# Kernel tuning notes

Hardware: AMD Instinct MI355X
Metric: run time of the kernel (lower is better)

The kernel has to match this reference:

```python
import jax, jax.numpy as jnp
import numpy as np

DIM = 64
NUM_HEAD = 4
C_IN = 2 * DIM                      # dim * proj_ratio
N_PER_HEAD = C_IN // NUM_HEAD       # 32
M_TRI = N_PER_HEAD * (N_PER_HEAD + 1) // 2   # 528
C_POOL = NUM_HEAD * M_TRI           # 2112 == dim*(dim+2)/2
EPS = 1e-5


def setup_inputs() -> dict:
    key = jax.random.key(0)
    ks = jax.random.split(key, 8)
    B, H, W = 4, 128, 128
    x = jax.random.normal(ks[0], (B, C_IN, H, W), dtype=jnp.float32)
    norm1_w = 1.0 + 0.1 * jax.random.normal(ks[1], (C_IN,), dtype=jnp.float32)
    norm1_b = 0.1 * jax.random.normal(ks[2], (C_IN,), dtype=jnp.float32)
    dr_w = 0.02 * jax.random.normal(ks[3], (DIM, C_POOL), dtype=jnp.float32)
    dr_b = 0.02 * jax.random.normal(ks[4], (DIM,), dtype=jnp.float32)
    norm2_w = 1.0 + 0.1 * jax.random.normal(ks[5], (DIM,), dtype=jnp.float32)
    norm2_b = 0.1 * jax.random.normal(ks[6], (DIM,), dtype=jnp.float32)
    fc1_w = 0.05 * jax.random.normal(ks[7], (DIM, DIM), dtype=jnp.float32)
    fc1_b = jnp.zeros((DIM,), dtype=jnp.float32)
    return {"x": x, "norm1_w": norm1_w, "norm1_b": norm1_b,
            "dr_w": dr_w, "dr_b": dr_b,
            "norm2_w": norm2_w, "norm2_b": norm2_b,
            "fc1_w": fc1_w, "fc1_b": fc1_b}


def _layernorm_nchw(x, g, b):
    # LayerNorm over channel dim of NCHW tensor (torch permutes to NHWC first)
    xt = jnp.transpose(x, (0, 2, 3, 1))
    mu = jnp.mean(xt, axis=-1, keepdims=True)
    var = jnp.mean(jnp.square(xt - mu), axis=-1, keepdims=True)
    y = (xt - mu) / jnp.sqrt(var + EPS) * g + b
    return jnp.transpose(y, (0, 3, 1, 2))


def reference(x, norm1_w, norm1_b, dr_w, dr_b, norm2_w, norm2_b, fc1_w, fc1_b):
    B, C, H, W = x.shape
    L = H * W
    nh, n = NUM_HEAD, N_PER_HEAD

    # --- norm1 ---
    x = _layernorm_nchw(x, norm1_w, norm1_b)

    # --- MHSP ---
    # channel shuffle: group = C // num_head = n, group_C = num_head
    x = x.reshape(B, n, nh, H, W).transpose(0, 2, 1, 3, 4).reshape(B, C, H, W)
    # unfold with kernel=1, stride=1, pad=0 is a pure reshape -> [B, L, C]
    t = x.reshape(B, C, L).transpose(0, 2, 1).reshape(B, L, nh, n)
    # per-position per-head rank-1 outer product: [B, L, nh, n, n]
    outer = jnp.einsum('blhi,blhj->blhij', t, t)
    # sparse_mapping matmul == gather of upper-triangle entries (row-major i<=j)
    iu, ju = np.triu_indices(n)
    pf = outer[..., iu, ju]                      # [B, L, nh, m]
    pf = pf.reshape(B, L, nh * M_TRI).transpose(0, 2, 1).reshape(B, C_POOL, H, W)

    # --- CTM token mixer ---
    C2 = C_POOL
    y = pf.reshape(B, nh, C2 // nh, L)
    yn = y / jnp.linalg.norm(y, axis=2, keepdims=True)
    mid = L // 2
    x0 = yn[..., mid]                            # [B, nh, C2/nh]
    attn = jnp.einsum('bhc,bhcl->bhl', x0, yn)   # [B, nh, L]
    attn = jax.nn.softmax(attn, axis=-1)[:, :, None, :]
    y = (y * attn * float(L)).reshape(B, C2, H, W)

    # --- dimension reduction (1x1 conv) ---
    z = jnp.einsum('bchw,oc->bohw', y, dr_w) + dr_b[None, :, None, None]

    # --- norm2 + LightMlp (1x1 conv + GELU) ---
    z = _layernorm_nchw(z, norm2_w, norm2_b)
    z = jnp.einsum('bchw,oc->bohw', z, fc1_w) + fc1_b[None, :, None, None]
    z = jax.nn.gelu(z, approximate=False)
    return z
```

## Files before the change

### kernel.cpp

```cpp
#include <hip/hip_runtime.h>
#include <hip/hip_bf16.h>
#include <math.h>

#define B_    4
#define CIN   128
#define L_    16384
#define NH    4
#define NN    32
#define MT    528
#define CP    2112
#define DIM_  64
#define LT    64
#define MID   8192
#define EPS_  1e-5f

#define KPH   640
#define KTOT  2560
#define WSWN  (KTOT * DIM_)
#define FSWN  (2 * 4 * 64 * 8)
#define LOGITS_BLOCKS 1024
#define PREP_BLOCKS   656

typedef __attribute__((ext_vector_type(8))) short short8;
typedef __attribute__((ext_vector_type(4))) float float4v;

__device__ inline unsigned short f2bf(float f) {
  unsigned u = __float_as_uint(f);
  unsigned r = (u + 0x7fffu + ((u >> 16) & 1u)) >> 16;
  return (unsigned short)r;
}
__device__ inline float bf2f(unsigned short h) {
  return __uint_as_float(((unsigned)h) << 16);
}

__device__ inline void kb_decode(int id, int& i, int& jb) {
  if (id < 32)      { i = id >> 2;               jb = id & 3; }
  else if (id < 56) { int r = id - 32; int d = r / 3; i = 8 + d;  jb = 1 + (r - 3 * d); }
  else if (id < 72) { int r = id - 56; i = 16 + (r >> 1); jb = 2 + (r & 1); }
  else              { i = 24 + (id - 72);         jb = 3; }
}

__global__ __launch_bounds__(256) void k_pre(const float* __restrict__ dr_w,
                                             const float* __restrict__ fc1_w,
                                             const float* __restrict__ x,
                                             const float* __restrict__ g1,
                                             const float* __restrict__ b1,
                                             unsigned short* __restrict__ wsw,
                                             unsigned short* __restrict__ fsw,
                                             float* __restrict__ ws_a,
                                             float* __restrict__ ws_bsum) {
  if (blockIdx.x >= LOGITS_BLOCKS) {
    int s = (blockIdx.x - LOGITS_BLOCKS) * 256 + threadIdx.x;
    if (s < WSWN) {
      int j    = s & 7;
      int lane = (s >> 3) & 63;
      int ot   = (s >> 9) & 3;
      int ksg  = s >> 11;
      int o  = ot * 16 + (lane & 15);
      int kp = ksg * 32 + (lane >> 4) * 8 + j;
      int h  = kp / KPH;
      int kk = kp - h * KPH;
      int kb = kk >> 3, jo = kk & 7;
      int i, jb; kb_decode(kb, i, jb);
      int jch = jb * 8 + jo;
      float val = 0.f;
      if (jch >= i) {
        int fi = 32 * i - (i * (i - 1)) / 2;
        int m  = h * MT + fi + (jch - i);
        val = dr_w[(size_t)o * CP + m];
      }
      wsw[s] = f2bf(val);
    } else {
      int s2 = s - WSWN;
      int j    = s2 & 7;
      int lane = (s2 >> 3) & 63;
      int ot   = (s2 >> 9) & 3;
      int ks2  = s2 >> 11;
      int o = ot * 16 + (lane & 15);
      int c = ks2 * 32 + (lane >> 4) * 8 + j;
      fsw[s2] = f2bf(fc1_w[o * DIM_ + c]);
    }
    return;
  }
  int blk = blockIdx.x;
  int b = blk >> 8;
  int l0 = (blk & 255) << 6;
  int t = threadIdx.x;
  int l = t & 63, q = t >> 6;
  __shared__ float xs[CIN], smid[CIN];
  __shared__ float part[4][64], part2[4][64], mu_s[64], isd_s[64];
  __shared__ float musd[2];

  if (t < CIN) xs[t] = x[(size_t)b * CIN * L_ + (size_t)t * L_ + MID];

  float tv[32];
  const float* xb = x + (size_t)b * CIN * L_ + l0 + l;
  float s = 0.f, s2 = 0.f;
#pragma unroll
  for (int cc = 0; cc < 32; cc++) {
    float v = xb[(size_t)(cc * 4 + q) * L_];
    tv[cc] = v; s += v; s2 += v * v;
  }
  part[q][l] = s; part2[q][l] = s2;
  __syncthreads();
  if (t == 0) {
    float su = 0.f;
    for (int c = 0; c < CIN; c++) su += xs[c];
    float mu = su / CIN;
    float sv = 0.f;
    for (int c = 0; c < CIN; c++) { float d = xs[c] - mu; sv += d * d; }
    musd[0] = mu; musd[1] = rsqrtf(sv / CIN + EPS_);
  }
  if (t < 64) {
    float su = part[0][t] + part[1][t] + part[2][t] + part[3][t];
    float su2 = part2[0][t] + part2[1][t] + part2[2][t] + part2[3][t];
    float mu = su * (1.f / CIN);
    float var = su2 * (1.f / CIN) - mu * mu;
    mu_s[t] = mu; isd_s[t] = rsqrtf(var + EPS_);
  }
  __syncthreads();
  if (t < CIN) {
    int c = ((t & 31) << 2) + (t >> 5);
    smid[t] = (xs[c] - musd[0]) * musd[1] * g1[c] + b1[c];
  }
  {
    float mu = mu_s[l], isd = isd_s[l];
#pragma unroll
    for (int cc = 0; cc < 32; cc++) {
      int co = cc * 4 + q;
      tv[cc] = (tv[cc] - mu) * isd * g1[co] + b1[co];
    }
  }
  __syncthreads();
  float T2 = 0.f, T4 = 0.f, st = 0.f, sc2 = 0.f, S2 = 0.f, S4 = 0.f;
#pragma unroll
  for (int i = 0; i < 32; i++) {
    float si = smid[q * 32 + i];
    float ti = tv[i];
    float t2 = ti * ti;
    T2 += t2; T4 = fmaf(t2, t2, T4);
    float ci = si * ti;
    st += ci; sc2 = fmaf(ci, ci, sc2);
    float s2i = si * si;
    S2 += s2i; S4 = fmaf(s2i, s2i, S4);
  }
  float num = 0.5f * (st * st + sc2);
  float logit = num * rsqrtf(0.25f * (T2 * T2 + T4) * (S2 * S2 + S4));
  float e = expf(logit - 1.f);
  ws_a[((size_t)b * NH + q) * L_ + l0 + l] = e;
  float ws = e;
#pragma unroll
  for (int mk = 1; mk < 64; mk <<= 1) ws += __shfl_xor(ws, mk, 64);
  if (l == 0) ws_bsum[((size_t)b * NH + q) * 256 + (blk & 255)] = ws;
}

struct __align__(16) SmemM {
  union __align__(16) { unsigned short p2[4 * 5 * 4 * 16 * 8]; float zb[64 * 65]; } u1;
  union __align__(16) { unsigned short ut[64 * 128]; unsigned short zn2[4 * 2 * 4 * 16 * 8]; } u2;
  float part[4][64], part2[4][64], mu_s[64], isd_s[64];
};

__device__ inline int utidx(int l, int c) {
  return l * 128 + ((((c >> 3) ^ (l & 7))) << 3) + (c & 7);
}

__global__ __launch_bounds__(256, 3) void k_main(const float* __restrict__ x,
      const float* __restrict__ g1, const float* __restrict__ b1,
      const float* __restrict__ dr_b,
      const float* __restrict__ g2, const float* __restrict__ b2,
      const float* __restrict__ fc1_b,
      const unsigned short* __restrict__ wsw, const unsigned short* __restrict__ fsw,
      const float* __restrict__ ws_a, const float* __restrict__ ws_bsum,
      float* __restrict__ out) {
  __shared__ SmemM sm;
  int blk = blockIdx.x;
  int b = blk >> 8;
  int l0 = (blk & 255) << 6;
  int t = threadIdx.x;
  int l = t & 63, q = t >> 6;

  float asum;
  {
    const float* bs = ws_bsum + ((size_t)b * NH + q) * 256;
    float a0 = bs[l] + bs[l + 64] + bs[l + 128] + bs[l + 192];
#pragma unroll
    for (int mk = 1; mk < 64; mk <<= 1) a0 += __shfl_xor(a0, mk, 64);
    asum = a0;
  }
  float e = ws_a[((size_t)b * NH + q) * L_ + l0 + l];
  float sa = sqrtf(e * ((float)L_ / asum));

  const float* xb = x + (size_t)b * CIN * L_ + l0;
  float s = 0.f, s2 = 0.f;
#pragma unroll
  for (int cb = 0; cb < 4; cb++) {
    unsigned short pk[8];
#pragma unroll
    for (int e8 = 0; e8 < 8; e8++) {
      int cc = cb * 8 + e8;
      int co = cc * 4 + q;
      float v = xb[(size_t)co * L_ + l];
      s += v; s2 += v * v;
      pk[e8] = f2bf(v);
    }
    *(short8*)&sm.u2.ut[l * 128 + (((q * 4 + cb) ^ (l & 7)) << 3)] = *(short8*)pk;
  }
  sm.part[q][l] = s; sm.part2[q][l] = s2;
  __syncthreads();
  if (t < 64) {
    float su = sm.part[0][t] + sm.part[1][t] + sm.part[2][t] + sm.part[3][t];
    float su2 = sm.part2[0][t] + sm.part2[1][t] + sm.part2[2][t] + sm.part2[3][t];
    float mu = su * (1.f / CIN);
    float var = su2 * (1.f / CIN) - mu * mu;
    sm.mu_s[t] = mu; sm.isd_s[t] = rsqrtf(var + EPS_);
  }
  __syncthreads();
  {
    float mu = sm.mu_s[l], isd = sm.isd_s[l];
#pragma unroll
    for (int cb = 0; cb < 4; cb++) {
      unsigned short* pp = &sm.u2.ut[l * 128 + (((q * 4 + cb) ^ (l & 7)) << 3)];
      short8 v8 = *(short8*)pp;
      unsigned short pk[8];
#pragma unroll
      for (int e8 = 0; e8 < 8; e8++) {
        int cc = cb * 8 + e8;
        int co = cc * 4 + q;
        float tvv = (bf2f((unsigned short)v8[e8]) - mu) * isd * g1[co] + b1[co];
        pk[e8] = f2bf(tvv * sa);
      }
      *(short8*)pp = *(short8*)pk;
    }
  }
  __syncthreads();

  const int otp = q & 1, ltp = q >> 1;
  const int lta = ltp * 2, ltb = ltp * 2 + 1;
  float4v acc[2][2];
  acc[0][0] = (float4v)0.f; acc[0][1] = (float4v)0.f;
  acc[1][0] = (float4v)0.f; acc[1][1] = (float4v)0.f;
  int tl = l;
  int ltile = l >> 4, n = l & 15;

  for (int cc16 = 0; cc16 < 16; cc16++) {
    int h = cc16 >> 2;
    int cpart = cc16 & 3;
#pragma unroll
    for (int s5 = 0; s5 < 5; s5++) {
      int kbl = q * 5 + s5;
      int kbh = cpart * 20 + kbl;
      int i, jb; kb_decode(kbh, i, jb);
      float ui = bf2f(sm.u2.ut[utidx(l, h * 32 + i)]);
      short8 ub = *(short8*)&sm.u2.ut[l * 128 + (((h * 4 + jb) ^ (l & 7)) << 3)];
      unsigned short pk[8];
#pragma unroll
      for (int e8 = 0; e8 < 8; e8++) pk[e8] = f2bf(ui * bf2f((unsigned short)ub[e8]));
      int ks = kbl >> 2, quad = kbl & 3;
      *(short8*)&sm.u1.p2[(((ltile * 5 + ks) * 4 + quad) * 16 + n) * 8] = *(short8*)pk;
    }
    __syncthreads();
#pragma unroll
    for (int ks = 0; ks < 5; ks++) {
      const unsigned short* wk = wsw + (size_t)(cc16 * 5 + ks) * 2048 + otp * 1024 + tl * 8;
      short8 a0 = *(const short8*)(wk);
      short8 a1 = *(const short8*)(wk + 512);
      short8 b0 = *(short8*)&sm.u1.p2[((lta * 5 + ks) * 64 + tl) * 8];
      short8 b1v = *(short8*)&sm.u1.p2[((ltb * 5 + ks) * 64 + tl) * 8];
      acc[0][0] = __builtin_amdgcn_mfma_f32_16x16x32_bf16(a0, b0,  acc[0][0], 0, 0, 0);
      acc[0][1] = __builtin_amdgcn_mfma_f32_16x16x32_bf16(a0, b1v, acc[0][1], 0, 0, 0);
      acc[1][0] = __builtin_amdgcn_mfma_f32_16x16x32_bf16(a1, b0,  acc[1][0], 0, 0, 0);
      acc[1][1] = __builtin_amdgcn_mfma_f32_16x16x32_bf16(a1, b1v, acc[1][1], 0, 0, 0);
    }
    __syncthreads();
  }

  int quad = tl >> 4;
#pragma unroll
  for (int oi = 0; oi < 2; oi++) {
#pragma unroll
    for (int li = 0; li < 2; li++) {
      int ot = otp * 2 + oi, ltx = ltp * 2 + li;
#pragma unroll
      for (int r = 0; r < 4; r++) {
        int o = ot * 16 + quad * 4 + r;
        sm.u1.zb[(ltx * 16 + n) * 65 + o] = acc[oi][li][r] + dr_b[o];
      }
    }
  }
  __syncthreads();
  {
    float ss = 0.f, ss2 = 0.f;
#pragma unroll
    for (int k = 0; k < 16; k++) {
      float v = sm.u1.zb[l * 65 + q * 16 + k];
      ss += v; ss2 += v * v;
    }
    sm.part[q][l] = ss; sm.part2[q][l] = ss2;
  }
  __syncthreads();
  if (t < 64) {
    float su = sm.part[0][t] + sm.part[1][t] + sm.part[2][t] + sm.part[3][t];
    float su2 = sm.part2[0][t] + sm.part2[1][t] + sm.part2[2][t] + sm.part2[3][t];
    float mu = su * (1.f / DIM_);
    float var = su2 * (1.f / DIM_) - mu * mu;
    sm.mu_s[t] = mu; sm.isd_s[t] = rsqrtf(var + EPS_);
  }
  __syncthreads();
  {
    float mu2 = sm.mu_s[l], isd2 = sm.isd_s[l];
#pragma unroll
    for (int kk = 0; kk < 2; kk++) {
      int kb2 = q * 2 + kk;
      int c0 = kb2 * 8;
      unsigned short pk[8];
#pragma unroll
      for (int e8 = 0; e8 < 8; e8++) {
        int c = c0 + e8;
        float v = (sm.u1.zb[l * 65 + c] - mu2) * isd2 * g2[c] + b2[c];
        pk[e8] = f2bf(v);
      }
      int ks2 = kb2 >> 2, qd2 = kb2 & 3;
      *(short8*)&sm.u2.zn2[(((ltile * 2 + ks2) * 4 + qd2) * 16 + n) * 8] = *(short8*)pk;
    }
  }
  __syncthreads();
  float4v acc2[4];
  acc2[0] = (float4v)0.f; acc2[1] = (float4v)0.f; acc2[2] = (float4v)0.f; acc2[3] = (float4v)0.f;
#pragma unroll
  for (int ks2 = 0; ks2 < 2; ks2++) {
    short8 bz = *(short8*)&sm.u2.zn2[((q * 2 + ks2) * 64 + tl) * 8];
    const unsigned short* fk = fsw + ks2 * 2048 + tl * 8;
    short8 f0 = *(const short8*)(fk);
    short8 f1 = *(const short8*)(fk + 512);
    short8 f2 = *(const short8*)(fk + 1024);
    short8 f3 = *(const short8*)(fk + 1536);
    acc2[0] = __builtin_amdgcn_mfma_f32_16x16x32_bf16(f0, bz, acc2[0], 0, 0, 0);
    acc2[1] = __builtin_amdgcn_mfma_f32_16x16x32_bf16(f1, bz, acc2[1], 0, 0, 0);
    acc2[2] = __builtin_amdgcn_mfma_f32_16x16x32_bf16(f2, bz, acc2[2], 0, 0, 0);
    acc2[3] = __builtin_amdgcn_mfma_f32_16x16x32_bf16(f3, bz, acc2[3], 0, 0, 0);
  }
#pragma unroll
  for (int ot = 0; ot < 4; ot++) {
#pragma unroll
    for (int r = 0; r < 4; r++) {
      int o2 = ot * 16 + quad * 4 + r;
      float sv = acc2[ot][r] + fc1_b[o2];
      float g = 0.5f * sv * (1.f + erff(sv * 0.70710678118f));
      out[((size_t)b * DIM_ + o2) * L_ + l0 + q * 16 + n] = g;
    }
  }
}

extern "C" void kernel_launch(void* const* d_in, const int* in_sizes, int n_in,
                              void* d_out, int out_size, void* d_ws, size_t ws_size,
                              hipStream_t stream) {
  const float* x    = (const float*)d_in[0];
  const float* n1w  = (const float*)d_in[1];
  const float* n1b  = (const float*)d_in[2];
  const float* drw  = (const float*)d_in[3];
  const float* drb  = (const float*)d_in[4];
  const float* n2w  = (const float*)d_in[5];
  const float* n2b  = (const float*)d_in[6];
  const float* fc1w = (const float*)d_in[7];
  const float* fc1b = (const float*)d_in[8];
  float* out = (float*)d_out;
  float* ws = (float*)d_ws;
  float* ws_a    = ws;
  float* ws_bsum = ws_a + (size_t)B_ * NH * L_;
  unsigned short* wsw = (unsigned short*)(ws_bsum + B_ * NH * 256);
  unsigned short* fsw = wsw + WSWN;

  hipLaunchKernelGGL(k_pre, dim3(LOGITS_BLOCKS + PREP_BLOCKS), dim3(256), 0, stream,
                     drw, fc1w, x, n1w, n1b, wsw, fsw, ws_a, ws_bsum);
  hipLaunchKernelGGL(k_main, dim3(B_ * (L_ / LT)), dim3(256), 0, stream,
                     x, n1w, n1b, drb, n2w, n2b, fc1b, wsw, fsw, ws_a, ws_bsum, out);
}
```

Baseline: 153.9 us.

## Keep normalized head channels in registers and rebuild weight layout per head

Each wave now holds its own head's 32 normalized channels in registers instead of staging all 128 channels through shared memory. The K dimension of the pooled GEMM is reordered so that each wave's quad maps to one head, and the pre-swizzled weight layout is rebuilt to match. This removes the shared-memory tile and one barrier, uses packed bf16 conversion, and raises the occupancy hint from 3 to 4 blocks. The cost is a larger register footprint (32 floats per thread plus full unrolling), which may spill or undercut the higher occupancy target.

```diff
diff --git a/kernel.cpp b/kernel.cpp
--- a/kernel.cpp
+++ b/kernel.cpp
@@ -57,12 +57,9 @@
       int ot   = (s >> 9) & 3;
       int ksg  = s >> 11;
       int o  = ot * 16 + (lane & 15);
-      int kp = ksg * 32 + (lane >> 4) * 8 + j;
-      int h  = kp / KPH;
-      int kk = kp - h * KPH;
-      int kb = kk >> 3, jo = kk & 7;
-      int i, jb; kb_decode(kb, i, jb);
-      int jch = jb * 8 + jo;
+      int h  = lane >> 4;
+      int i, jb; kb_decode(ksg, i, jb);
+      int jch = jb * 8 + j;
       float val = 0.f;
       if (jch >= i) {
         int fi = 32 * i - (i * (i - 1)) / 2;
@@ -156,15 +153,11 @@
 
 struct __align__(16) SmemM {
   union __align__(16) { unsigned short p2[4 * 5 * 4 * 16 * 8]; float zb[64 * 65]; } u1;
-  union __align__(16) { unsigned short ut[64 * 128]; unsigned short zn2[4 * 2 * 4 * 16 * 8]; } u2;
+  unsigned short zn2[4 * 2 * 4 * 16 * 8];
   float part[4][64], part2[4][64], mu_s[64], isd_s[64];
 };
 
-__device__ inline int utidx(int l, int c) {
-  return l * 128 + ((((c >> 3) ^ (l & 7))) << 3) + (c & 7);
-}
-
-__global__ __launch_bounds__(256, 3) void k_main(const float* __restrict__ x,
+__global__ __launch_bounds__(256, 4) void k_main(const float* __restrict__ x,
       const float* __restrict__ g1, const float* __restrict__ b1,
       const float* __restrict__ dr_b,
       const float* __restrict__ g2, const float* __restrict__ b2,
@@ -190,20 +183,13 @@
   float e = ws_a[((size_t)b * NH + q) * L_ + l0 + l];
   float sa = sqrtf(e * ((float)L_ / asum));
 
-  const float* xb = x + (size_t)b * CIN * L_ + l0;
+  const float* xb = x + (size_t)b * CIN * L_ + l0 + l;
+  float tn[32];
   float s = 0.f, s2 = 0.f;
 #pragma unroll
-  for (int cb = 0; cb < 4; cb++) {
-    unsigned short pk[8];
-#pragma unroll
-    for (int e8 = 0; e8 < 8; e8++) {
-      int cc = cb * 8 + e8;
-      int co = cc * 4 + q;
-      float v = xb[(size_t)co * L_ + l];
-      s += v; s2 += v * v;
-      pk[e8] = f2bf(v);
-    }
-    *(short8*)&sm.u2.ut[l * 128 + (((q * 4 + cb) ^ (l & 7)) << 3)] = *(short8*)pk;
+  for (int cc = 0; cc < 32; cc++) {
+    float v = xb[(size_t)(cc * 4 + q) * L_];
+    tn[cc] = v; s += v; s2 += v * v;
   }
   sm.part[q][l] = s; sm.part2[q][l] = s2;
   __syncthreads();
@@ -218,21 +204,11 @@
   {
     float mu = sm.mu_s[l], isd = sm.isd_s[l];
 #pragma unroll
-    for (int cb = 0; cb < 4; cb++) {
-      unsigned short* pp = &sm.u2.ut[l * 128 + (((q * 4 + cb) ^ (l & 7)) << 3)];
-      short8 v8 = *(short8*)pp;
-      unsigned short pk[8];
-#pragma unroll
-      for (int e8 = 0; e8 < 8; e8++) {
-        int cc = cb * 8 + e8;
-        int co = cc * 4 + q;
-        float tvv = (bf2f((unsigned short)v8[e8]) - mu) * isd * g1[co] + b1[co];
-        pk[e8] = f2bf(tvv * sa);
-      }
-      *(short8*)pp = *(short8*)pk;
-    }
-  }
-  __syncthreads();
+    for (int cc = 0; cc < 32; cc++) {
+      int co = cc * 4 + q;
+      tn[cc] = ((tn[cc] - mu) * isd * g1[co] + b1[co]) * sa;
+    }
+  }
 
   const int otp = q & 1, ltp = q >> 1;
   const int lta = ltp * 2, ltb = ltp * 2 + 1;
@@ -242,26 +218,26 @@
   int tl = l;
   int ltile = l >> 4, n = l & 15;
 
-  for (int cc16 = 0; cc16 < 16; cc16++) {
-    int h = cc16 >> 2;
-    int cpart = cc16 & 3;
-#pragma unroll
-    for (int s5 = 0; s5 < 5; s5++) {
-      int kbl = q * 5 + s5;
-      int kbh = cpart * 20 + kbl;
-      int i, jb; kb_decode(kbh, i, jb);
-      float ui = bf2f(sm.u2.ut[utidx(l, h * 32 + i)]);
-      short8 ub = *(short8*)&sm.u2.ut[l * 128 + (((h * 4 + jb) ^ (l & 7)) << 3)];
-      unsigned short pk[8];
-#pragma unroll
-      for (int e8 = 0; e8 < 8; e8++) pk[e8] = f2bf(ui * bf2f((unsigned short)ub[e8]));
-      int ks = kbl >> 2, quad = kbl & 3;
-      *(short8*)&sm.u1.p2[(((ltile * 5 + ks) * 4 + quad) * 16 + n) * 8] = *(short8*)pk;
+#pragma unroll
+  for (int p = 0; p < 16; p++) {
+#pragma unroll
+    for (int ks = 0; ks < 5; ks++) {
+      int g = p * 5 + ks;
+      int i, jb; kb_decode(g, i, jb);
+      float ui = tn[i];
+      union { unsigned u[4]; short8 v; } pk;
+#pragma unroll
+      for (int e2 = 0; e2 < 4; e2++) {
+        float f0 = tn[jb * 8 + e2 * 2] * ui;
+        float f1 = tn[jb * 8 + e2 * 2 + 1] * ui;
+        asm("v_cvt_pk_bf16_f32 %0, %1, %2" : "=v"(pk.u[e2]) : "v"(f0), "v"(f1));
+      }
+      *(short8*)&sm.u1.p2[(((ltile * 5 + ks) * 4 + q) * 16 + n) * 8] = pk.v;
     }
     __syncthreads();
 #pragma unroll
     for (int ks = 0; ks < 5; ks++) {
-      const unsigned short* wk = wsw + (size_t)(cc16 * 5 + ks) * 2048 + otp * 1024 + tl * 8;
+      const unsigned short* wk = wsw + (size_t)(p * 5 + ks) * 2048 + otp * 1024 + tl * 8;
       short8 a0 = *(const short8*)(wk);
       short8 a1 = *(const short8*)(wk + 512);
       short8 b0 = *(short8*)&sm.u1.p2[((lta * 5 + ks) * 64 + tl) * 8];
@@ -320,7 +296,7 @@
         pk[e8] = f2bf(v);
       }
       int ks2 = kb2 >> 2, qd2 = kb2 & 3;
-      *(short8*)&sm.u2.zn2[(((ltile * 2 + ks2) * 4 + qd2) * 16 + n) * 8] = *(short8*)pk;
+      *(short8*)&sm.zn2[(((ltile * 2 + ks2) * 4 + qd2) * 16 + n) * 8] = *(short8*)pk;
     }
   }
   __syncthreads();
@@ -328,7 +304,7 @@
   acc2[0] = (float4v)0.f; acc2[1] = (float4v)0.f; acc2[2] = (float4v)0.f; acc2[3] = (float4v)0.f;
 #pragma unroll
   for (int ks2 = 0; ks2 < 2; ks2++) {
-    short8 bz = *(short8*)&sm.u2.zn2[((q * 2 + ks2) * 64 + tl) * 8];
+    short8 bz = *(short8*)&sm.zn2[((q * 2 + ks2) * 64 + tl) * 8];
     const unsigned short* fk = fsw + ks2 * 2048 + tl * 8;
     short8 f0 = *(const short8*)(fk);
     short8 f1 = *(const short8*)(fk + 512);
```

New measurement: 169.4 us. +10.1%, slower.
